# Performance work log

Measured on AMD Instinct MI355X. Metric: run time of the kernel, lower is better.

Reference implementation:

```python
import jax, jax.numpy as jnp
import numpy as np

B, S, D = 2, 2048, 1024
H, DH = 16, 64
IGNORE = -100000.0
ATTN_SCALE = float(np.sqrt(DH))


def setup_inputs() -> dict:
    key = jax.random.key(0)
    ks = jax.random.split(key, 9)
    sc = 0.02
    return {
        "x": jax.random.normal(ks[0], (B, S, D), dtype=jnp.float32),
        "W_Q": jax.random.normal(ks[1], (H, DH, D), dtype=jnp.float32) * sc,
        "W_K": jax.random.normal(ks[2], (H, DH, D), dtype=jnp.float32) * sc,
        "W_V": jax.random.normal(ks[3], (H, DH, D), dtype=jnp.float32) * sc,
        "W_O": jax.random.normal(ks[4], (H, D, DH), dtype=jnp.float32) * sc,
        "b_Q": jax.random.normal(ks[5], (H, DH), dtype=jnp.float32) * sc,
        "b_K": jax.random.normal(ks[6], (H, DH), dtype=jnp.float32) * sc,
        "b_V": jax.random.normal(ks[7], (H, DH), dtype=jnp.float32) * sc,
        "b_O": jax.random.normal(ks[8], (D,), dtype=jnp.float32) * sc,
    }


def reference(x, W_Q, W_K, W_V, W_O, b_Q, b_K, b_V, b_O):
    # QKV projections: [b, pos, head, d_head]
    q = jnp.einsum('ihm,bpm->bpih', W_Q, x) + b_Q
    k = jnp.einsum('ihm,bpm->bpih', W_K, x) + b_K
    v = jnp.einsum('ihm,bpm->bpih', W_V, x) + b_V
    # scores[b, head, query_pos, key_pos]
    scores = jnp.einsum('bpih,bqih->bipq', q, k) / ATTN_SCALE
    Sq = x.shape[1]
    causal = jnp.tril(jnp.ones((Sq, Sq), dtype=bool))  # global causal mask
    scores = jnp.where(causal, scores, jnp.float32(IGNORE))
    attn = jax.nn.softmax(scores, axis=-1)
    # z[b, query_pos, head, d_head]
    z = jnp.einsum('bpih,biqp->bqih', v, attn)
    out = jnp.einsum('idh,bqih->bqd', W_O, z) + b_O
    return out
```

## Files before the change

### kernel.cpp

```cpp
#include <hip/hip_runtime.h>
#include <stdint.h>

typedef __attribute__((ext_vector_type(8))) short short8;
typedef __attribute__((ext_vector_type(4))) float f32x4;

#define AS1(p) ((const __attribute__((address_space(1))) void*)(p))
#define AS3(p) ((__attribute__((address_space(3))) void*)(p))

__device__ __forceinline__ void gload_lds16(const void* g, void* l) {
  __builtin_amdgcn_global_load_lds(AS1(g), AS3(l), 16, 0, 0);
}

__device__ __forceinline__ uint32_t cvtpk_bf16(float a, float b) {
  uint32_t d;
  asm("v_cvt_pk_bf16_f32 %0, %1, %2" : "=v"(d) : "v"(a), "v"(b));
  return d;
}

__device__ __forceinline__ float fast_exp2(float x) {
#if __has_builtin(__builtin_amdgcn_exp2f)
  return __builtin_amdgcn_exp2f(x);
#else
  return exp2f(x);
#endif
}

#define QSCALE 0.1803368801111244f

__global__ void cast_x_k(const float* __restrict__ in, uint2* __restrict__ out) {
  int i = blockIdx.x * 256 + threadIdx.x;
  float4 v = ((const float4*)in)[i];
  uint2 o;
  o.x = cvtpk_bf16(v.x, v.y);
  o.y = cvtpk_bf16(v.z, v.w);
  out[i] = o;
}

__global__ void cast_wqkv_k(const float* __restrict__ wq, const float* __restrict__ wk,
                            const float* __restrict__ wv, uint2* __restrict__ out) {
  int i = blockIdx.x * 256 + threadIdx.x;
  int e = i * 4;
  const float* src = (e < (1 << 20)) ? (wq + e)
                   : (e < (2 << 20)) ? (wk + (e - (1 << 20)))
                                     : (wv + (e - (2 << 20)));
  float4 v = *(const float4*)src;
  uint2 o;
  o.x = cvtpk_bf16(v.x, v.y);
  o.y = cvtpk_bf16(v.z, v.w);
  out[i] = o;
}

__global__ void cast_wo_k(const float* __restrict__ wo, uint2* __restrict__ out) {
  int i = blockIdx.x * 256 + threadIdx.x;
  int o4 = i * 4;
  int d = o4 >> 10, c = o4 & 1023;
  const float* s = wo + ((c >> 6) << 16) + (d << 6) + (c & 63);
  float4 v = *(const float4*)s;
  uint2 o;
  o.x = cvtpk_bf16(v.x, v.y);
  o.y = cvtpk_bf16(v.z, v.w);
  out[i] = o;
}

__global__ void bias_k(const float* __restrict__ bq, const float* __restrict__ bk,
                       const float* __restrict__ bv, float* __restrict__ out) {
  int i = blockIdx.x * 256 + threadIdx.x;
  out[i] = (i < 1024) ? bq[i] : (i < 2048) ? bk[i - 1024] : bv[i - 2048];
}

template <int EPI>
__global__ __launch_bounds__(256) void gemm_bt(const short* __restrict__ A,
                                               const short* __restrict__ Bm,
                                               const float* __restrict__ bias,
                                               void* __restrict__ Cout, int K, int ldc) {
  __shared__ short As[128 * 32];
  __shared__ short Bs[128 * 32];
  const int t = threadIdx.x;
  const int l = t & 63, w = t >> 6;
  const int wr = w >> 1, wc = w & 1;
  const int q = l & 15, g = l >> 4;
  const long brow = (long)blockIdx.y * 128;
  const long bcol = (long)blockIdx.x * 128;
  f32x4 acc[4][4] = {};
  const int r4 = t >> 2, cb = (t & 3) * 8;
  const short* aptr = A + (brow + r4) * (long)K + cb;
  const short* bptr = Bm + (bcol + r4) * (long)K + cb;
  for (int k0 = 0; k0 < K; k0 += 32) {
    gload_lds16(aptr + k0, &As[r4 * 32 + cb]);
    gload_lds16(aptr + k0 + 64 * (long)K, &As[(r4 + 64) * 32 + cb]);
    gload_lds16(bptr + k0, &Bs[r4 * 32 + cb]);
    gload_lds16(bptr + k0 + 64 * (long)K, &Bs[(r4 + 64) * 32 + cb]);
    __syncthreads();
    short8 af[4], bfr[4];
#pragma unroll
    for (int m = 0; m < 4; ++m)
      af[m] = *(const short8*)&As[(wr * 64 + m * 16 + q) * 32 + g * 8];
#pragma unroll
    for (int n = 0; n < 4; ++n)
      bfr[n] = *(const short8*)&Bs[(wc * 64 + n * 16 + q) * 32 + g * 8];
#pragma unroll
    for (int m = 0; m < 4; ++m)
#pragma unroll
      for (int n = 0; n < 4; ++n)
        acc[m][n] = __builtin_amdgcn_mfma_f32_16x16x32_bf16(af[m], bfr[n], acc[m][n], 0, 0, 0);
    __syncthreads();
  }
#pragma unroll
  for (int m = 0; m < 4; ++m)
#pragma unroll
    for (int n = 0; n < 4; ++n)
#pragma unroll
      for (int r = 0; r < 4; ++r) {
        long row = brow + wr * 64 + m * 16 + g * 4 + r;
        long col = bcol + wc * 64 + n * 16 + q;
        float v = acc[m][n][r] + bias[col];
        if (EPI == 0) {
          if (col < 1024) v *= QSCALE;
          ((unsigned short*)Cout)[row * ldc + col] = (unsigned short)cvtpk_bf16(v, v);
        } else {
          ((float*)Cout)[row * ldc + col] = v;
        }
      }
}

__global__ __launch_bounds__(256) void attn(const short* __restrict__ qkv,
                                            unsigned short* __restrict__ zb) {
  __shared__ short Ks[2][64 * 64];
  __shared__ short Vt[64 * 64];
  __shared__ unsigned short Ps[8][16 * 64];
  const int bid = blockIdx.x;
  const int r_ = bid >> 7;
  const int u_ = (bid >> 3) & 15;
  const int x_ = bid & 7;
  const int bh = r_ * 8 + x_;
  const int pr = (r_ < 2) ? u_ : 15 - u_;
  const int qtA = 31 - pr, qtB = pr;
  const int b = bh >> 4, h = bh & 15;
  const int t = threadIdx.x, l = t & 63, w = t >> 6;
  const int lq = l & 15, g = l >> 4;
  const int u = t >> 3, c8 = t & 7;
  const long rowbase = (long)b * 2048;
  const short* qp = qkv + rowbase * 3072 + h * 64;
  const short* kp = qp + 1024;
  const short* vp = qp + 2048;

  short8 qfA[2], qfB[2];
#pragma unroll
  for (int kg = 0; kg < 2; ++kg) {
    qfA[kg] = *(const short8*)(qp + (long)(qtA * 64 + w * 16 + lq) * 3072 + kg * 32 + g * 8);
    qfB[kg] = *(const short8*)(qp + (long)(qtB * 64 + w * 16 + lq) * 3072 + kg * 32 + g * 8);
  }
  f32x4 zA[4] = {}, zB[4] = {};
  float mA = -1e30f, lA = 0.0f, mB = -1e30f, lB = 0.0f;

  auto step = [&](const short* ksb, unsigned short* Pw, f32x4 (&zacc)[4],
                  float& mrun, float& lrun, short8 (&qf)[2], bool diag) {
    f32x4 sacc[4] = {};
#pragma unroll
    for (int m = 0; m < 4; ++m) {
#pragma unroll
      for (int kg = 0; kg < 2; ++kg) {
        int krow = m * 16 + lq;
        int blk = kg * 4 + g;
        short8 kf = *(const short8*)&ksb[krow * 64 + (blk ^ (krow & 7)) * 8];
        sacc[m] = __builtin_amdgcn_mfma_f32_16x16x32_bf16(kf, qf[kg], sacc[m], 0, 0, 0);
      }
    }
    if (diag) {
#pragma unroll
      for (int m = 0; m < 4; ++m)
#pragma unroll
        for (int r = 0; r < 4; ++r)
          if (m * 16 + g * 4 + r > w * 16 + lq) sacc[m][r] = -1e30f;
    }
    float red[8];
#pragma unroll
    for (int i2 = 0; i2 < 8; ++i2)
      red[i2] = fmaxf(sacc[i2 >> 2][i2 & 3], sacc[2 + (i2 >> 2)][i2 & 3]);
#pragma unroll
    for (int i2 = 0; i2 < 4; ++i2) red[i2] = fmaxf(red[i2], red[i2 + 4]);
    float mx = fmaxf(fmaxf(red[0], red[2]), fmaxf(red[1], red[3]));
    mx = fmaxf(mx, __shfl_xor(mx, 16));
    mx = fmaxf(mx, __shfl_xor(mx, 32));
    if (!__all(mx <= mrun + 8.0f)) {
      float mnew = fmaxf(mrun, mx);
      float alpha = fast_exp2(mrun - mnew);
      lrun *= alpha;
#pragma unroll
      for (int r = 0; r < 4; ++r) {
        float ar = __shfl(alpha, g * 4 + r);
#pragma unroll
        for (int n2 = 0; n2 < 4; ++n2) zacc[n2][r] *= ar;
      }
      mrun = mnew;
    }
#pragma unroll
    for (int m = 0; m < 4; ++m)
#pragma unroll
      for (int r = 0; r < 4; ++r) sacc[m][r] = fast_exp2(sacc[m][r] - mrun);
    float rs[8];
#pragma unroll
    for (int i2 = 0; i2 < 8; ++i2)
      rs[i2] = sacc[i2 >> 2][i2 & 3] + sacc[2 + (i2 >> 2)][i2 & 3];
#pragma unroll
    for (int i2 = 0; i2 < 4; ++i2) rs[i2] = rs[i2] + rs[i2 + 4];
    float ts = (rs[0] + rs[2]) + (rs[1] + rs[3]);
    ts += __shfl_xor(ts, 16);
    ts += __shfl_xor(ts, 32);
    lrun += ts;
#pragma unroll
    for (int m = 0; m < 4; ++m) {
      uint2 wv;
      wv.x = cvtpk_bf16(sacc[m][0], sacc[m][1]);
      wv.y = cvtpk_bf16(sacc[m][2], sacc[m][3]);
      int c = m * 4 + g;
      int csw = c ^ ((lq & 7) << 1);
      *(uint2*)&Pw[lq * 64 + csw * 4] = wv;
    }
    short8 pf[2];
#pragma unroll
    for (int kg2 = 0; kg2 < 2; ++kg2) {
      int c0 = kg2 * 8 + g * 2;
      int c0s = c0 ^ ((lq & 7) << 1);
      pf[kg2] = *(const short8*)&Pw[lq * 64 + c0s * 4];
    }
#pragma unroll
    for (int n2 = 0; n2 < 4; ++n2) {
#pragma unroll
      for (int kg2 = 0; kg2 < 2; ++kg2) {
        int dh = n2 * 16 + lq;
        int sw = (dh & 7) ^ ((dh >> 3) & 7);
        int blk = kg2 * 4 + g;
        short8 vf = *(const short8*)&Vt[dh * 64 + ((blk ^ sw) * 8)];
        zacc[n2] = __builtin_amdgcn_mfma_f32_16x16x32_bf16(pf[kg2], vf, zacc[n2], 0, 0, 0);
      }
    }
  };

  auto stageK = [&](int tile, int buf) {
#pragma unroll
    for (int i = 0; i < 2; ++i) {
      int r = i * 32 + u;
      int cbk = (c8 ^ (r & 7)) * 8;
      gload_lds16(kp + (long)(tile * 64 + r) * 3072 + cbk, &Ks[buf][i * 2048 + t * 8]);
    }
  };

  short8 va0, va1;
  {
    stageK(0, 0);
    const short* vrow = vp + (long)(2 * u) * 3072 + c8 * 8;
    va0 = *(const short8*)vrow;
    va1 = *(const short8*)(vrow + 3072);
  }

  for (int j = 0; j <= qtA; ++j) {
    const int buf = j & 1;
    asm volatile("s_waitcnt vmcnt(0)" ::: "memory");
    __builtin_amdgcn_sched_barrier(0);
    __builtin_amdgcn_s_barrier();
    {
      int blk = u >> 2, rl = (u & 3) * 2;
#pragma unroll
      for (int idx = 0; idx < 8; ++idx) {
        int dh = c8 * 8 + idx;
        int sw = (dh & 7) ^ ((dh >> 3) & 7);
        uint32_t pk = (uint32_t)(uint16_t)va0[idx] | ((uint32_t)(uint16_t)va1[idx] << 16);
        *(uint32_t*)&Vt[dh * 64 + ((blk ^ sw) * 8) + rl] = pk;
      }
    }
    if (j < qtA) {
      stageK(j + 1, buf ^ 1);
      const short* vrow = vp + (long)((j + 1) * 64 + 2 * u) * 3072 + c8 * 8;
      va0 = *(const short8*)vrow;
      va1 = *(const short8*)(vrow + 3072);
    }
    asm volatile("s_waitcnt lgkmcnt(0)" ::: "memory");
    __builtin_amdgcn_sched_barrier(0);
    __builtin_amdgcn_s_barrier();
    step(&Ks[buf][0], &Ps[w][0], zA, mA, lA, qfA, j == qtA);
    if (j <= qtB)
      step(&Ks[buf][0], &Ps[4 + w][0], zB, mB, lB, qfB, j == qtB);
  }

  auto wout = [&](f32x4 (&zacc)[4], float lrun, int qt) {
#pragma unroll
    for (int r = 0; r < 4; ++r) {
      float linv = 1.0f / __shfl(lrun, g * 4 + r);
      long grow = rowbase + qt * 64 + w * 16 + g * 4 + r;
#pragma unroll
      for (int n2 = 0; n2 < 4; ++n2) {
        int col = h * 64 + n2 * 16 + lq;
        float zv = zacc[n2][r] * linv;
        zb[grow * 1024 + col] = (unsigned short)cvtpk_bf16(zv, zv);
      }
    }
  };
  wout(zA, lA, qtA);
  wout(zB, lB, qtB);
}

extern "C" void kernel_launch(void* const* d_in, const int* in_sizes, int n_in,
                              void* d_out, int out_size, void* d_ws, size_t ws_size,
                              hipStream_t stream) {
  const float* x  = (const float*)d_in[0];
  const float* wq = (const float*)d_in[1];
  const float* wk = (const float*)d_in[2];
  const float* wv = (const float*)d_in[3];
  const float* wo = (const float*)d_in[4];
  const float* bq = (const float*)d_in[5];
  const float* bk = (const float*)d_in[6];
  const float* bv = (const float*)d_in[7];
  const float* bo = (const float*)d_in[8];
  char* ws = (char*)d_ws;
  if (ws_size < ((size_t)48 * 1024 * 1024 + 16384)) return;
  short*          xb    = (short*)(ws);
  short*          qkvb  = (short*)(ws + ((size_t)8  << 20));
  unsigned short* zbuf  = (unsigned short*)(ws + ((size_t)32 << 20));
  short*          wqkvb = (short*)(ws + ((size_t)40 << 20));
  short*          mob   = (short*)(ws + ((size_t)46 << 20));
  float*          bqkv  = (float*)(ws + ((size_t)48 << 20));

  cast_x_k   <<<4096, 256, 0, stream>>>(x, (uint2*)xb);
  cast_wqkv_k<<<3072, 256, 0, stream>>>(wq, wk, wv, (uint2*)wqkvb);
  cast_wo_k  <<<1024, 256, 0, stream>>>(wo, (uint2*)mob);
  bias_k     <<<12,   256, 0, stream>>>(bq, bk, bv, bqkv);

  gemm_bt<0><<<dim3(24, 32), 256, 0, stream>>>(xb, wqkvb, bqkv, (void*)qkvb, 1024, 3072);
  attn      <<<512,          256, 0, stream>>>(qkvb, zbuf);
  gemm_bt<1><<<dim3(8, 32),  256, 0, stream>>>((const short*)zbuf, mob, bo, d_out, 1024, 1024);
}
```

Before: 131.8 us.

## Double-buffer GEMM LDS tiles and raise wave priority around MFMA blocks

The projection GEMM now keeps two LDS buffers per operand. It issues the global-to-LDS load for the next K-slice before computing on the current one, and drops one of the two barriers per iteration. Separately, s_setprio is raised around the MFMA sequences in both the GEMM and the attention step so that waves in their matrix phase get issue priority over waves doing softmax or loads. The intent is to hide global load latency and improve MFMA/VALU interleaving, at the cost of doubled LDS use in the GEMM, which may reduce occupancy.

```diff
diff --git a/kernel.cpp b/kernel.cpp
--- a/kernel.cpp
+++ b/kernel.cpp
@@ -73,8 +73,8 @@
                                                const short* __restrict__ Bm,
                                                const float* __restrict__ bias,
                                                void* __restrict__ Cout, int K, int ldc) {
-  __shared__ short As[128 * 32];
-  __shared__ short Bs[128 * 32];
+  __shared__ short As[2][128 * 32];
+  __shared__ short Bs[2][128 * 32];
   const int t = threadIdx.x;
   const int l = t & 63, w = t >> 6;
   const int wr = w >> 1, wc = w & 1;
@@ -85,25 +85,33 @@
   const int r4 = t >> 2, cb = (t & 3) * 8;
   const short* aptr = A + (brow + r4) * (long)K + cb;
   const short* bptr = Bm + (bcol + r4) * (long)K + cb;
+  auto stage = [&](int k0, int buf) {
+    gload_lds16(aptr + k0, &As[buf][r4 * 32 + cb]);
+    gload_lds16(aptr + k0 + 64 * (long)K, &As[buf][(r4 + 64) * 32 + cb]);
+    gload_lds16(bptr + k0, &Bs[buf][r4 * 32 + cb]);
+    gload_lds16(bptr + k0 + 64 * (long)K, &Bs[buf][(r4 + 64) * 32 + cb]);
+  };
+  stage(0, 0);
+  __syncthreads();
+  int cur = 0;
   for (int k0 = 0; k0 < K; k0 += 32) {
-    gload_lds16(aptr + k0, &As[r4 * 32 + cb]);
-    gload_lds16(aptr + k0 + 64 * (long)K, &As[(r4 + 64) * 32 + cb]);
-    gload_lds16(bptr + k0, &Bs[r4 * 32 + cb]);
-    gload_lds16(bptr + k0 + 64 * (long)K, &Bs[(r4 + 64) * 32 + cb]);
-    __syncthreads();
+    if (k0 + 32 < K) stage(k0 + 32, cur ^ 1);
     short8 af[4], bfr[4];
 #pragma unroll
     for (int m = 0; m < 4; ++m)
-      af[m] = *(const short8*)&As[(wr * 64 + m * 16 + q) * 32 + g * 8];
+      af[m] = *(const short8*)&As[cur][(wr * 64 + m * 16 + q) * 32 + g * 8];
 #pragma unroll
     for (int n = 0; n < 4; ++n)
-      bfr[n] = *(const short8*)&Bs[(wc * 64 + n * 16 + q) * 32 + g * 8];
+      bfr[n] = *(const short8*)&Bs[cur][(wc * 64 + n * 16 + q) * 32 + g * 8];
+    __builtin_amdgcn_s_setprio(1);
 #pragma unroll
     for (int m = 0; m < 4; ++m)
 #pragma unroll
       for (int n = 0; n < 4; ++n)
         acc[m][n] = __builtin_amdgcn_mfma_f32_16x16x32_bf16(af[m], bfr[n], acc[m][n], 0, 0, 0);
-    __syncthreads();
+    __builtin_amdgcn_s_setprio(0);
+    if (k0 + 32 < K) __syncthreads();
+    cur ^= 1;
   }
 #pragma unroll
   for (int m = 0; m < 4; ++m)
@@ -156,6 +164,7 @@
   auto step = [&](const short* ksb, unsigned short* Pw, f32x4 (&zacc)[4],
                   float& mrun, float& lrun, short8 (&qf)[2], bool diag) {
     f32x4 sacc[4] = {};
+    __builtin_amdgcn_s_setprio(1);
 #pragma unroll
     for (int m = 0; m < 4; ++m) {
 #pragma unroll
@@ -166,6 +175,7 @@
         sacc[m] = __builtin_amdgcn_mfma_f32_16x16x32_bf16(kf, qf[kg], sacc[m], 0, 0, 0);
       }
     }
+    __builtin_amdgcn_s_setprio(0);
     if (diag) {
 #pragma unroll
       for (int m = 0; m < 4; ++m)
@@ -224,6 +234,7 @@
       int c0s = c0 ^ ((lq & 7) << 1);
       pf[kg2] = *(const short8*)&Pw[lq * 64 + c0s * 4];
     }
+    __builtin_amdgcn_s_setprio(1);
 #pragma unroll
     for (int n2 = 0; n2 < 4; ++n2) {
 #pragma unroll
@@ -235,6 +246,7 @@
         zacc[n2] = __builtin_amdgcn_mfma_f32_16x16x32_bf16(pf[kg2], vf, zacc[n2], 0, 0, 0);
       }
     }
+    __builtin_amdgcn_s_setprio(0);
   };
 
   auto stageK = [&](int tile, int buf) {
```

After: 161.9 us. 1.23x slower.

## Double GEMM K-tile to 64 with XOR-swizzled LDS layout

Applied to the files above, without the earlier changes.

The projection GEMM now stages a 64-wide K slice per iteration instead of 32, which halves the number of barrier pairs per K loop and doubles MFMA work per sync. The LDS tile is stored with an XOR swizzle on 16-byte chunks so that fragment reads across rows avoid bank conflicts at the wider row stride. The trailing barrier is skipped on the last iteration. In exchange, LDS usage per block doubles, which may reduce occupancy, and K must be a multiple of 64.

```diff
diff --git a/kernel.cpp b/kernel.cpp
--- a/kernel.cpp
+++ b/kernel.cpp
@@ -73,8 +73,8 @@
                                                const short* __restrict__ Bm,
                                                const float* __restrict__ bias,
                                                void* __restrict__ Cout, int K, int ldc) {
-  __shared__ short As[128 * 32];
-  __shared__ short Bs[128 * 32];
+  __shared__ short As[128 * 64];
+  __shared__ short Bs[128 * 64];
   const int t = threadIdx.x;
   const int l = t & 63, w = t >> 6;
   const int wr = w >> 1, wc = w & 1;
@@ -82,28 +82,37 @@
   const long brow = (long)blockIdx.y * 128;
   const long bcol = (long)blockIdx.x * 128;
   f32x4 acc[4][4] = {};
-  const int r4 = t >> 2, cb = (t & 3) * 8;
-  const short* aptr = A + (brow + r4) * (long)K + cb;
-  const short* bptr = Bm + (bcol + r4) * (long)K + cb;
-  for (int k0 = 0; k0 < K; k0 += 32) {
-    gload_lds16(aptr + k0, &As[r4 * 32 + cb]);
-    gload_lds16(aptr + k0 + 64 * (long)K, &As[(r4 + 64) * 32 + cb]);
-    gload_lds16(bptr + k0, &Bs[r4 * 32 + cb]);
-    gload_lds16(bptr + k0 + 64 * (long)K, &Bs[(r4 + 64) * 32 + cb]);
+  const int r8 = t >> 3;
+  const int sc8 = (t & 7) ^ (r8 & 7);
+  const short* aptr = A + (brow + r8) * (long)K + sc8 * 8;
+  const short* bptr = Bm + (bcol + r8) * (long)K + sc8 * 8;
+  const int qs = q & 7;
+  for (int k0 = 0; k0 < K; k0 += 64) {
+#pragma unroll
+    for (int c = 0; c < 4; ++c) {
+      gload_lds16(aptr + k0 + c * 32 * (long)K, &As[(c * 256 + t) * 8]);
+      gload_lds16(bptr + k0 + c * 32 * (long)K, &Bs[(c * 256 + t) * 8]);
+    }
     __syncthreads();
-    short8 af[4], bfr[4];
+    short8 af[4][2], bfr[4][2];
 #pragma unroll
     for (int m = 0; m < 4; ++m)
-      af[m] = *(const short8*)&As[(wr * 64 + m * 16 + q) * 32 + g * 8];
+#pragma unroll
+      for (int kk = 0; kk < 2; ++kk)
+        af[m][kk] = *(const short8*)&As[(wr * 64 + m * 16 + q) * 64 + ((kk * 4 + g) ^ qs) * 8];
 #pragma unroll
     for (int n = 0; n < 4; ++n)
-      bfr[n] = *(const short8*)&Bs[(wc * 64 + n * 16 + q) * 32 + g * 8];
+#pragma unroll
+      for (int kk = 0; kk < 2; ++kk)
+        bfr[n][kk] = *(const short8*)&Bs[(wc * 64 + n * 16 + q) * 64 + ((kk * 4 + g) ^ qs) * 8];
 #pragma unroll
     for (int m = 0; m < 4; ++m)
 #pragma unroll
-      for (int n = 0; n < 4; ++n)
-        acc[m][n] = __builtin_amdgcn_mfma_f32_16x16x32_bf16(af[m], bfr[n], acc[m][n], 0, 0, 0);
-    __syncthreads();
+      for (int n = 0; n < 4; ++n) {
+        acc[m][n] = __builtin_amdgcn_mfma_f32_16x16x32_bf16(af[m][0], bfr[n][0], acc[m][n], 0, 0, 0);
+        acc[m][n] = __builtin_amdgcn_mfma_f32_16x16x32_bf16(af[m][1], bfr[n][1], acc[m][n], 0, 0, 0);
+      }
+    if (k0 + 64 < K) __syncthreads();
   }
 #pragma unroll
   for (int m = 0; m < 4; ++m)
```

Measured after the change: 117.0 us. 11.2% less time.
